# Performance work log

Hardware: AMD Instinct MI355X
Metric: run time of the kernel (lower is better)

Reference implementation:

```python
import jax, jax.numpy as jnp
import numpy as np
import math

N_HEADS = 16
D_EFF = 64
ROPE_BASE = 500.0


def _rope(x, cos, sin):
    # x: (b, h, L, d_eff); cos/sin: (L, d_eff//2)
    x_even = x[..., 0::2]
    x_odd = x[..., 1::2]
    rot = jnp.stack([x_even * cos - x_odd * sin,
                     x_even * sin + x_odd * cos], axis=-1)
    return rot.reshape(x.shape)


def setup_inputs() -> dict:
    key = jax.random.key(0)
    ks = jax.random.split(key, 5)
    B, L, D = 1, 2048, 1024
    X = jax.random.normal(ks[0], (B, L, D), dtype=jnp.float32)
    # causal mask (1 = keep, 0 = masked), broadcastable to (B, h, L, L)
    mask = jnp.tril(jnp.ones((L, L), dtype=jnp.int32))[None, :, :]
    s = 1.0 / math.sqrt(D)
    Wq = jax.random.normal(ks[1], (D, D), dtype=jnp.float32) * s
    Wk = jax.random.normal(ks[2], (D, D), dtype=jnp.float32) * s
    Wv = jax.random.normal(ks[3], (D, D), dtype=jnp.float32) * s
    Wo = jax.random.normal(ks[4], (D, D), dtype=jnp.float32) * s
    return {"X": X, "mask": mask, "Wq": Wq, "Wk": Wk, "Wv": Wv, "Wo": Wo}


def reference(X, mask, Wq, Wk, Wv, Wo):
    b, L, d_model = X.shape
    h, d = N_HEADS, D_EFF
    d_full = h * d

    def split_heads(Y):
        return Y.reshape(b, L, h, d).transpose(0, 2, 1, 3)  # (b,h,L,d)

    Q = split_heads(X @ Wq)
    K = split_heads(X @ Wk)
    V = split_heads(X @ Wv)

    # interleaved RoPE, base 500
    inv_freq = 1.0 / (ROPE_BASE ** (jnp.arange(0, d, 2, dtype=jnp.float32) / d))
    freqs = jnp.arange(L, dtype=jnp.float32)[:, None] * inv_freq  # (L, d/2)
    cos, sin = jnp.cos(freqs), jnp.sin(freqs)
    Q = _rope(Q, cos, sin)
    K = _rope(K, cos, sin)

    S = jnp.einsum('bhqd,bhkd->bhqk', Q, K) / math.sqrt(d)
    S = jnp.where(mask[:, None, :, :] == 0, jnp.float32(-1e9), S)
    # NOTE: faithful to original torch code: softmax over the HEADS axis (dim=1)
    A = jax.nn.softmax(S, axis=1)
    Y = jnp.einsum('bhqk,bhkd->bhqd', A, V)
    Y = Y.transpose(0, 2, 1, 3).reshape(b, L, d_full)
    Y = Y @ Wo
    return Y * math.sqrt(d_model / d_full)
```

## Files before the change

kernel.cpp:

```cpp
#include <hip/hip_runtime.h>
#include <stdint.h>
#include <stddef.h>
#include <math.h>

typedef __attribute__((ext_vector_type(8))) short bf16x8;
typedef __attribute__((ext_vector_type(4))) short short4v;
typedef __attribute__((ext_vector_type(4))) float f32x4;

__device__ __forceinline__ short f2bf(float f) {
  union { float f; uint32_t u; } x; x.f = f;
  return (short)((x.u + 0x7fffu + ((x.u >> 16) & 1u)) >> 16);
}
__device__ __forceinline__ float bf2f(short s) {
  union { uint32_t u; float f; } x; x.u = ((uint32_t)(uint16_t)s) << 16;
  return x.f;
}
__device__ __forceinline__ uint32_t cvt_pk_bf16(float a, float b) {
  uint32_t r;
  asm("v_cvt_pk_bf16_f32 %0, %1, %2" : "=v"(r) : "v"(a), "v"(b));
  return r;
}

__device__ __forceinline__ void gload_lds16(const void* g, void* lds) {
  __builtin_amdgcn_global_load_lds(
      (const __attribute__((address_space(1))) void*)g,
      (__attribute__((address_space(3))) void*)lds, 16, 0, 0);
}

__global__ __launch_bounds__(256) void cast_b(const float* __restrict__ s,
                                              short* __restrict__ d,
                                              float* __restrict__ Cvs) {
  if (blockIdx.x == 0) {
    int c4 = threadIdx.x * 4;
    Cvs[c4] = 0.f; Cvs[c4 + 1] = 0.f; Cvs[c4 + 2] = 0.f; Cvs[c4 + 3] = 0.f;
  }
  int i4 = (blockIdx.x * 256 + threadIdx.x) * 4;
  float4 v = *(const float4*)&s[i4];
  short4v r = { f2bf(v.x), f2bf(v.y), f2bf(v.z), f2bf(v.w) };
  *(short4v*)&d[i4] = r;
}

__global__ __launch_bounds__(256) void reduce_y(const short* __restrict__ Ypc,
                                                const float* __restrict__ Cvs,
                                                short* __restrict__ o) {
  int q = blockIdx.x;
  int j = q >> 5, qr = q & 31;
  int col = threadIdx.x * 4;
  float a0 = Cvs[col + 0], a1 = Cvs[col + 1], a2 = Cvs[col + 2], a3 = Cvs[col + 3];
  int cf = (j - 2) >> 2;
  for (int c = 0; c <= cf; c++) {
    int slot = (c <= 7) ? (c + 8 * (j - 4 * c - 2)) : ((15 - c) + 8 * j);
    const short* p = Ypc + ((size_t)slot * 32 + qr) * 1024 + col;
    short4v v = *(const short4v*)p;
    a0 += bf2f(v[0]); a1 += bf2f(v[1]); a2 += bf2f(v[2]); a3 += bf2f(v[3]);
  }
  if ((j & 3) < 2) {
    int cp = j >> 2;
    int slot = (cp <= 7) ? (cp + 8 * (64 + (j & 3)))
                         : ((15 - cp) + 8 * (66 + (j & 3)));
    const short* p = Ypc + ((size_t)slot * 32 + qr) * 1024 + col;
    short4v v = *(const short4v*)p;
    a0 += bf2f(v[0]); a1 += bf2f(v[1]); a2 += bf2f(v[2]); a3 += bf2f(v[3]);
  }
  uint32_t u0 = cvt_pk_bf16(a0, a1), u1 = cvt_pk_bf16(a2, a3);
  short4v rr = { (short)u0, (short)(u0 >> 16), (short)u1, (short)(u1 >> 16) };
  *(short4v*)&o[(size_t)q * 1024 + col] = rr;
}

__global__ __launch_bounds__(256) void transW(const float* __restrict__ Wq,
                                              const float* __restrict__ Wk,
                                              const float* __restrict__ Wv,
                                              const float* __restrict__ Wo,
                                              short* __restrict__ WcatT,
                                              short* __restrict__ WoT) {
  int z = blockIdx.z;
  const float* src = (z == 0) ? Wq : (z == 1) ? Wk : (z == 2) ? Wv : Wo;
  short* dst = (z == 3) ? WoT : WcatT + (size_t)z * 1024 * 1024;
  __shared__ float tl[32][33];
  int tx = threadIdx.x & 31, ty = threadIdx.x >> 5;
  int kk0 = blockIdx.x * 32;
  int nn0 = blockIdx.y * 32;
#pragma unroll
  for (int j = 0; j < 4; j++)
    tl[ty + j * 8][tx] = src[(size_t)(kk0 + ty + j * 8) * 1024 + nn0 + tx];
  __syncthreads();
#pragma unroll
  for (int j = 0; j < 4; j++)
    dst[(size_t)(nn0 + ty + j * 8) * 1024 + kk0 + tx] = f2bf(tl[tx][ty + j * 8]);
}

__global__ __launch_bounds__(256) void transpose_v(const short* __restrict__ Vb,
                                                   short* __restrict__ Vt,
                                                   float* __restrict__ Cvs) {
  __shared__ short tv[64][72];
  int h = blockIdx.y, k0 = blockIdx.x * 64;
  int tid = threadIdx.x;
#pragma unroll
  for (int j = 0; j < 2; j++) {
    int idx = tid + j * 256;
    int row = idx >> 3, c = idx & 7;
    bf16x8 v = *(const bf16x8*)&Vb[((size_t)h * 2048 + k0 + row) * 64 + c * 8];
#pragma unroll
    for (int t = 0; t < 8; t++) tv[row][c * 8 + t] = v[t];
  }
  __syncthreads();
#pragma unroll
  for (int j = 0; j < 2; j++) {
    int idx = tid + j * 256;
    int d = idx >> 3, c = idx & 7;
    bf16x8 v;
#pragma unroll
    for (int t = 0; t < 8; t++) v[t] = tv[c * 8 + t][d];
    *(bf16x8*)&Vt[((size_t)h * 64 + d) * 2048 + k0 + c * 8] = v;
  }
  if (tid < 64) {
    float s = 0.f;
#pragma unroll 8
    for (int k = 0; k < 64; k++) s += bf2f(tv[k][tid]);
    atomicAdd(&Cvs[h * 64 + tid], s * 0.0625f);
  }
}

template <int MODE>
__global__ __launch_bounds__(256, 2)
void gemm_kernel(const short* __restrict__ A, const short* __restrict__ B,
                 int N, int K, float* __restrict__ C,
                 short* __restrict__ Qb, short* __restrict__ Kb,
                 short* __restrict__ Vb) {
  __shared__ __attribute__((aligned(16))) short lga[128 * 64];
  __shared__ __attribute__((aligned(16))) short lgb[128 * 64];
  const int tid = threadIdx.x;
  const int lane = tid & 63;
  const int w = tid >> 6;
  const int l15 = lane & 15;
  const int quad = lane >> 4;
  const int wm = w >> 1, wn = w & 1;
  const int m0 = blockIdx.x * 128, n0 = blockIdx.y * 128;
  const int rsub = lane >> 3;
  const int cpos = lane & 7;

  f32x4 acc[4][4];
#pragma unroll
  for (int i = 0; i < 4; i++)
#pragma unroll
    for (int j = 0; j < 4; j++) acc[i][j] = (f32x4){0.f, 0.f, 0.f, 0.f};

  for (int kb = 0; kb < K; kb += 64) {
    __syncthreads();
#pragma unroll
    for (int j = 0; j < 4; j++) {
      int r = (w * 4 + j) * 8 + rsub;
      int kc = cpos ^ rsub;
      gload_lds16(A + (size_t)(m0 + r) * K + kb + kc * 8, &lga[(w * 4 + j) * 512]);
      gload_lds16(B + (size_t)(n0 + r) * K + kb + kc * 8, &lgb[(w * 4 + j) * 512]);
    }
    __syncthreads();
#pragma unroll
    for (int kk = 0; kk < 2; kk++) {
      bf16x8 af[4], bfr[4];
#pragma unroll
      for (int t = 0; t < 4; t++) {
        int row = wm * 64 + t * 16 + l15;
        int pc = (kk * 4 + quad) ^ (row & 7);
        af[t] = *(const bf16x8*)&lga[row * 64 + pc * 8];
        int rowb = wn * 64 + t * 16 + l15;
        int pcb = (kk * 4 + quad) ^ (rowb & 7);
        bfr[t] = *(const bf16x8*)&lgb[rowb * 64 + pcb * 8];
      }
#pragma unroll
      for (int mt = 0; mt < 4; mt++)
#pragma unroll
        for (int nt = 0; nt < 4; nt++)
          acc[mt][nt] = __builtin_amdgcn_mfma_f32_16x16x32_bf16(
              af[mt], bfr[nt], acc[mt][nt], 0, 0, 0);
    }
  }

  if (MODE == 0) {
#pragma unroll
    for (int mt = 0; mt < 4; mt++) {
      int q = m0 + wm * 64 + mt * 16 + quad * 4;
#pragma unroll
      for (int nt = 0; nt < 4; nt++) {
        int n = n0 + wn * 64 + nt * 16 + l15;
#pragma unroll
        for (int r = 0; r < 4; r++) C[(size_t)(q + r) * N + n] = acc[mt][nt][r];
      }
    }
  } else {
#pragma unroll
    for (int mt = 0; mt < 4; mt++) {
#pragma unroll
      for (int nt = 0; nt < 4; nt++) {
        int n = n0 + wn * 64 + nt * 16 + l15;
        int mat = n >> 10;
        int h = (n >> 6) & 15;
        int d = n & 63;
#pragma unroll
        for (int r = 0; r < 4; r++) {
          int q = m0 + wm * 64 + mt * 16 + quad * 4 + r;
          float v = acc[mt][nt][r];
          float o = __shfl_xor(v, 1, 64);
          if (mat < 2) {
            int i = d >> 1;
            float ang = (float)q * __builtin_exp2f(-(float)i * 0.2801807588956902f);
            float sn, cs;
            __sincosf(ang, &sn, &cs);
            float rv = (d & 1) ? (o * sn + v * cs) : (v * cs - o * sn);
            short* dst = (mat == 0) ? Qb : Kb;
            dst[((size_t)h * 2048 + q) * 64 + d] = f2bf(rv);
          } else {
            Vb[((size_t)h * 2048 + q) * 64 + d] = f2bf(v);
          }
        }
      }
    }
  }
}

__global__ __launch_bounds__(256, 4)
void gemm_o(const short* __restrict__ A, const short* __restrict__ B,
            float* __restrict__ C) {
  __shared__ __attribute__((aligned(16))) short lga[128 * 64];
  __shared__ __attribute__((aligned(16))) short lgb[64 * 64];
  const int tid = threadIdx.x;
  const int lane = tid & 63;
  const int w = tid >> 6;
  const int l15 = lane & 15;
  const int quad = lane >> 4;
  const int m0 = blockIdx.x * 128, n0 = blockIdx.y * 64;
  const int rsub = lane >> 3;
  const int cpos = lane & 7;

  f32x4 acc[2][4];
#pragma unroll
  for (int i = 0; i < 2; i++)
#pragma unroll
    for (int j = 0; j < 4; j++) acc[i][j] = (f32x4){0.f, 0.f, 0.f, 0.f};

  for (int kb = 0; kb < 1024; kb += 64) {
    __syncthreads();
    int kc = cpos ^ rsub;
#pragma unroll
    for (int j = 0; j < 4; j++) {
      int r = (w * 4 + j) * 8 + rsub;
      gload_lds16(A + (size_t)(m0 + r) * 1024 + kb + kc * 8, &lga[(w * 4 + j) * 512]);
    }
#pragma unroll
    for (int j = 0; j < 2; j++) {
      int r = (w * 2 + j) * 8 + rsub;
      gload_lds16(B + (size_t)(n0 + r) * 1024 + kb + kc * 8, &lgb[(w * 2 + j) * 512]);
    }
    __syncthreads();
#pragma unroll
    for (int kk = 0; kk < 2; kk++) {
      bf16x8 af[2], bfr[4];
#pragma unroll
      for (int t = 0; t < 2; t++) {
        int row = w * 32 + t * 16 + l15;
        int pc = (kk * 4 + quad) ^ (row & 7);
        af[t] = *(const bf16x8*)&lga[row * 64 + pc * 8];
      }
#pragma unroll
      for (int t = 0; t < 4; t++) {
        int rowb = t * 16 + l15;
        int pcb = (kk * 4 + quad) ^ (rowb & 7);
        bfr[t] = *(const bf16x8*)&lgb[rowb * 64 + pcb * 8];
      }
#pragma unroll
      for (int mt = 0; mt < 2; mt++)
#pragma unroll
        for (int nt = 0; nt < 4; nt++)
          acc[mt][nt] = __builtin_amdgcn_mfma_f32_16x16x32_bf16(
              af[mt], bfr[nt], acc[mt][nt], 0, 0, 0);
    }
  }

#pragma unroll
  for (int mt = 0; mt < 2; mt++) {
    int q = m0 + w * 32 + mt * 16 + quad * 4;
#pragma unroll
    for (int nt = 0; nt < 4; nt++) {
      int n = n0 + nt * 16 + l15;
#pragma unroll
      for (int r = 0; r < 4; r++) C[(size_t)(q + r) * 1024 + n] = acc[mt][nt][r];
    }
  }
}

__global__ __launch_bounds__(1024, 2)
void attn_kernel(const short* __restrict__ Qb, const short* __restrict__ Kb,
                 const short* __restrict__ Vt, short* __restrict__ Ypc) {
  __shared__ short Sb[16 * 32 * 72];
  const int tid = threadIdx.x;
  const int lane = tid & 63;
  const int h = tid >> 6;
  const int l15 = lane & 15, quad = lane >> 4;
  const int b = blockIdx.x;
  const int x = b & 7, s = b >> 3;
  int c, j, ng;
  const int n1 = 62 - 4 * x;
  if (s < n1)      { c = x;      j = 4 * x + 2 + s;        ng = 2; }
  else if (s < 64) { c = 15 - x; j = s;                    ng = 2; }
  else if (s < 66) { c = x;      j = 4 * x + (s - 64);     ng = 1; }
  else             { c = 15 - x; j = 60 - 4 * x + (s - 66); ng = 1; }
  const int q0 = j * 32;
  const int g0 = 2 * c;

  bf16x8 qf[2][2];
#pragma unroll
  for (int qs = 0; qs < 2; qs++)
#pragma unroll
    for (int cc = 0; cc < 2; cc++)
      qf[qs][cc] = *(const bf16x8*)&Qb[((size_t)h * 2048 + q0 + qs * 16 + l15) * 64 +
                                       cc * 32 + quad * 8];

  f32x4 yacc[2][4];
#pragma unroll
  for (int i = 0; i < 2; i++)
#pragma unroll
    for (int jj = 0; jj < 4; jj++) yacc[i][jj] = (f32x4){0.f, 0.f, 0.f, 0.f};

  for (int gi = 0; gi < ng; gi++) {
    const int k0 = (g0 + gi) * 64;
#pragma unroll
    for (int st = 0; st < 4; st++) {
      const short* kb = &Kb[((size_t)h * 2048 + k0 + st * 16 + l15) * 64 + quad * 8];
      bf16x8 kf0 = *(const bf16x8*)kb;
      bf16x8 kf1 = *(const bf16x8*)(kb + 32);
#pragma unroll
      for (int qs = 0; qs < 2; qs++) {
        f32x4 sa = (f32x4){0.f, 0.f, 0.f, 0.f};
        sa = __builtin_amdgcn_mfma_f32_16x16x32_bf16(qf[qs][0], kf0, sa, 0, 0, 0);
        sa = __builtin_amdgcn_mfma_f32_16x16x32_bf16(qf[qs][1], kf1, sa, 0, 0, 0);
        const float cs = 0.18033688011112042f;
        uint32_t u0 = cvt_pk_bf16(sa[0] * cs, sa[1] * cs);
        uint32_t u1 = cvt_pk_bf16(sa[2] * cs, sa[3] * cs);
        int rb = (h * 32 + qs * 16 + quad * 4) * 72 + st * 16 + l15;
        Sb[rb]       = (short)u0;
        Sb[rb + 72]  = (short)(u0 >> 16);
        Sb[rb + 144] = (short)u1;
        Sb[rb + 216] = (short)(u1 >> 16);
      }
    }
    __syncthreads();
#pragma unroll
    for (int pp = 0; pp < 2; pp++) {
      int p = tid + pp * 1024;
      int q = p >> 6, kl = p & 63;
      int base = q * 72 + kl;
      float t[16];
      float sum = 0.f;
#pragma unroll
      for (int hh = 0; hh < 16; hh++) {
        float e = __builtin_exp2f(bf2f(Sb[hh * 2304 + base]));
        t[hh] = e;
        sum += e;
      }
      bool msk = (k0 + kl) > (q0 + q);
      float rs = msk ? 0.f : 1.f / sum;
      float offv = msk ? 0.f : 0.0625f;
#pragma unroll
      for (int hh = 0; hh < 16; hh += 2) {
        uint32_t u = cvt_pk_bf16(t[hh] * rs - offv, t[hh + 1] * rs - offv);
        Sb[hh * 2304 + base]       = (short)u;
        Sb[(hh + 1) * 2304 + base] = (short)(u >> 16);
      }
    }
    __syncthreads();
#pragma unroll
    for (int kk = 0; kk < 2; kk++) {
      bf16x8 af0 = *(const bf16x8*)&Sb[(h * 32 + l15) * 72 + kk * 32 + quad * 8];
      bf16x8 af1 = *(const bf16x8*)&Sb[(h * 32 + 16 + l15) * 72 + kk * 32 + quad * 8];
#pragma unroll
      for (int nt = 0; nt < 4; nt++) {
        bf16x8 vf = *(const bf16x8*)&Vt[((size_t)h * 64 + nt * 16 + l15) * 2048 +
                                        k0 + kk * 32 + quad * 8];
        yacc[0][nt] = __builtin_amdgcn_mfma_f32_16x16x32_bf16(af0, vf, yacc[0][nt],
                                                              0, 0, 0);
        yacc[1][nt] = __builtin_amdgcn_mfma_f32_16x16x32_bf16(af1, vf, yacc[1][nt],
                                                              0, 0, 0);
      }
    }
    __syncthreads();
  }
  short* Y = Ypc + (size_t)b * 32 * 1024;
#pragma unroll
  for (int qs = 0; qs < 2; qs++) {
#pragma unroll
    for (int nt = 0; nt < 4; nt++) {
      int col = h * 64 + nt * 16 + l15;
#pragma unroll
      for (int rr = 0; rr < 4; rr++)
        Y[(size_t)(qs * 16 + quad * 4 + rr) * 1024 + col] = f2bf(yacc[qs][nt][rr]);
    }
  }
}

extern "C" void kernel_launch(void* const* d_in, const int* in_sizes, int n_in,
                              void* d_out, int out_size, void* d_ws, size_t ws_size,
                              hipStream_t stream) {
  (void)in_sizes; (void)n_in; (void)out_size; (void)ws_size;
  const float* X  = (const float*)d_in[0];
  const float* Wq = (const float*)d_in[2];
  const float* Wk = (const float*)d_in[3];
  const float* Wv = (const float*)d_in[4];
  const float* Wo = (const float*)d_in[5];
  char* ws = (char*)d_ws;
  const size_t MB = 1024 * 1024;
  short* Xbf   = (short*)(ws + 0);
  short* WcatT = (short*)(ws + 4 * MB);
  short* WoT   = (short*)(ws + 10 * MB);
  short* Qb    = (short*)(ws + 12 * MB);
  short* Kb    = (short*)(ws + 16 * MB);
  short* Vb    = (short*)(ws + 20 * MB);
  short* Vt    = (short*)(ws + 24 * MB);
  short* Ypc   = (short*)(ws + 28 * MB);
  float* Cvs   = (float*)(ws + 63 * MB);
  short* Ycbf  = Xbf;
  float* out   = (float*)d_out;

  cast_b<<<dim3(2048), dim3(256), 0, stream>>>(X, Xbf, Cvs);
  transW<<<dim3(32, 32, 4), dim3(256), 0, stream>>>(Wq, Wk, Wv, Wo, WcatT, WoT);
  gemm_kernel<1><<<dim3(16, 24), dim3(256), 0, stream>>>(Xbf, WcatT, 3072, 1024,
                                                         nullptr, Qb, Kb, Vb);
  transpose_v<<<dim3(32, 16), dim3(256), 0, stream>>>(Vb, Vt, Cvs);
  attn_kernel<<<dim3(544), dim3(1024), 0, stream>>>(Qb, Kb, Vt, Ypc);
  reduce_y<<<dim3(2048), dim3(256), 0, stream>>>(Ypc, Cvs, Ycbf);
  gemm_o<<<dim3(16, 16), dim3(256), 0, stream>>>(Ycbf, WoT, out);
}
```

Measured before the change: 203.6 us.

## Repartition attention into 16-query blocks with 512 threads and 4-chunk key spans

Each attention block now covers 16 query rows instead of 32, using 512 threads where each wave handles two heads. Each block takes up to four 64-key chunks instead of two, and a new block-to-(query, chunk) schedule produces 576 blocks. The partial-output slot mapping and the reduction kernel are rewritten to match. The aim is smaller blocks with more occupancy per CU (launch bounds 512,4) and better load balance across the triangular causal work, at the cost of a different partial-sum count and index arithmetic.

```diff
diff --git a/kernel.cpp b/kernel.cpp
--- a/kernel.cpp
+++ b/kernel.cpp
@@ -44,22 +44,17 @@
                                                 const float* __restrict__ Cvs,
                                                 short* __restrict__ o) {
   int q = blockIdx.x;
-  int j = q >> 5, qr = q & 31;
+  int j = q >> 4, qr = q & 15;
   int col = threadIdx.x * 4;
   float a0 = Cvs[col + 0], a1 = Cvs[col + 1], a2 = Cvs[col + 2], a3 = Cvs[col + 3];
-  int cf = (j - 2) >> 2;
-  for (int c = 0; c <= cf; c++) {
-    int slot = (c <= 7) ? (c + 8 * (j - 4 * c - 2)) : ((15 - c) + 8 * j);
-    const short* p = Ypc + ((size_t)slot * 32 + qr) * 1024 + col;
-    short4v v = *(const short4v*)p;
-    a0 += bf2f(v[0]); a1 += bf2f(v[1]); a2 += bf2f(v[2]); a3 += bf2f(v[3]);
-  }
-  if ((j & 3) < 2) {
-    int cp = j >> 2;
-    int slot = (cp <= 7) ? (cp + 8 * (64 + (j & 3)))
-                         : ((15 - cp) + 8 * (66 + (j & 3)));
-    const short* p = Ypc + ((size_t)slot * 32 + qr) * 1024 + col;
-    short4v v = *(const short4v*)p;
+  int cmax = j >> 4;
+  for (int c = 0; c <= cmax; c++) {
+    int p, t;
+    if (c < 4) { p = c;     t = j - 16 * c; }
+    else       { p = 7 - c; t = j + 16; }
+    int slot = (2 * p + (t & 1)) + 8 * (71 - (t >> 1));
+    const short* pp = Ypc + ((size_t)slot * 16 + qr) * 1024 + col;
+    short4v v = *(const short4v*)pp;
     a0 += bf2f(v[0]); a1 += bf2f(v[1]); a2 += bf2f(v[2]); a3 += bf2f(v[3]);
   }
   uint32_t u0 = cvt_pk_bf16(a0, a1), u1 = cvt_pk_bf16(a2, a3);
@@ -288,31 +283,34 @@
   }
 }
 
-__global__ __launch_bounds__(1024, 2)
+__global__ __launch_bounds__(512, 4)
 void attn_kernel(const short* __restrict__ Qb, const short* __restrict__ Kb,
                  const short* __restrict__ Vt, short* __restrict__ Ypc) {
-  __shared__ short Sb[16 * 32 * 72];
+  __shared__ short Sb[16 * 16 * 72];
   const int tid = threadIdx.x;
   const int lane = tid & 63;
-  const int h = tid >> 6;
+  const int w = tid >> 6;
+  const int h0 = w * 2;
   const int l15 = lane & 15, quad = lane >> 4;
   const int b = blockIdx.x;
-  const int x = b & 7, s = b >> 3;
-  int c, j, ng;
-  const int n1 = 62 - 4 * x;
-  if (s < n1)      { c = x;      j = 4 * x + 2 + s;        ng = 2; }
-  else if (s < 64) { c = 15 - x; j = s;                    ng = 2; }
-  else if (s < 66) { c = x;      j = 4 * x + (s - 64);     ng = 1; }
-  else             { c = 15 - x; j = 60 - 4 * x + (s - 66); ng = 1; }
-  const int q0 = j * 32;
-  const int g0 = 2 * c;
+  const int x = b & 7;
+  const int p = x >> 1;
+  const int t = 2 * (71 - (b >> 3)) + (x & 1);
+  int c, j;
+  if (t < 128 - 16 * p) { c = p;     j = 16 * p + t; }
+  else                  { c = 7 - p; j = t - 16; }
+  const int G = (j >> 2) + 1;
+  const int g0 = 4 * c;
+  int ngt = G - g0;
+  const int ng = (ngt > 4) ? 4 : ngt;
+  const int q0 = j * 16;
 
   bf16x8 qf[2][2];
 #pragma unroll
-  for (int qs = 0; qs < 2; qs++)
+  for (int hh = 0; hh < 2; hh++)
 #pragma unroll
     for (int cc = 0; cc < 2; cc++)
-      qf[qs][cc] = *(const bf16x8*)&Qb[((size_t)h * 2048 + q0 + qs * 16 + l15) * 64 +
+      qf[hh][cc] = *(const bf16x8*)&Qb[((size_t)(h0 + hh) * 2048 + q0 + l15) * 64 +
                                        cc * 32 + quad * 8];
 
   f32x4 yacc[2][4];
@@ -324,19 +322,20 @@
   for (int gi = 0; gi < ng; gi++) {
     const int k0 = (g0 + gi) * 64;
 #pragma unroll
-    for (int st = 0; st < 4; st++) {
-      const short* kb = &Kb[((size_t)h * 2048 + k0 + st * 16 + l15) * 64 + quad * 8];
-      bf16x8 kf0 = *(const bf16x8*)kb;
-      bf16x8 kf1 = *(const bf16x8*)(kb + 32);
-#pragma unroll
-      for (int qs = 0; qs < 2; qs++) {
+    for (int hh = 0; hh < 2; hh++) {
+      int h = h0 + hh;
+#pragma unroll
+      for (int st = 0; st < 4; st++) {
+        const short* kb = &Kb[((size_t)h * 2048 + k0 + st * 16 + l15) * 64 + quad * 8];
+        bf16x8 kf0 = *(const bf16x8*)kb;
+        bf16x8 kf1 = *(const bf16x8*)(kb + 32);
         f32x4 sa = (f32x4){0.f, 0.f, 0.f, 0.f};
-        sa = __builtin_amdgcn_mfma_f32_16x16x32_bf16(qf[qs][0], kf0, sa, 0, 0, 0);
-        sa = __builtin_amdgcn_mfma_f32_16x16x32_bf16(qf[qs][1], kf1, sa, 0, 0, 0);
+        sa = __builtin_amdgcn_mfma_f32_16x16x32_bf16(qf[hh][0], kf0, sa, 0, 0, 0);
+        sa = __builtin_amdgcn_mfma_f32_16x16x32_bf16(qf[hh][1], kf1, sa, 0, 0, 0);
         const float cs = 0.18033688011112042f;
         uint32_t u0 = cvt_pk_bf16(sa[0] * cs, sa[1] * cs);
         uint32_t u1 = cvt_pk_bf16(sa[2] * cs, sa[3] * cs);
-        int rb = (h * 32 + qs * 16 + quad * 4) * 72 + st * 16 + l15;
+        int rb = (h * 16 + quad * 4) * 72 + st * 16 + l15;
         Sb[rb]       = (short)u0;
         Sb[rb + 72]  = (short)(u0 >> 16);
         Sb[rb + 144] = (short)u1;
@@ -346,15 +345,15 @@
     __syncthreads();
 #pragma unroll
     for (int pp = 0; pp < 2; pp++) {
-      int p = tid + pp * 1024;
-      int q = p >> 6, kl = p & 63;
+      int ppos = tid + pp * 512;
+      int q = ppos >> 6, kl = ppos & 63;
       int base = q * 72 + kl;
-      float t[16];
+      float tv[16];
       float sum = 0.f;
 #pragma unroll
       for (int hh = 0; hh < 16; hh++) {
-        float e = __builtin_exp2f(bf2f(Sb[hh * 2304 + base]));
-        t[hh] = e;
+        float e = __builtin_exp2f(bf2f(Sb[hh * 1152 + base]));
+        tv[hh] = e;
         sum += e;
       }
       bool msk = (k0 + kl) > (q0 + q);
@@ -362,37 +361,38 @@
       float offv = msk ? 0.f : 0.0625f;
 #pragma unroll
       for (int hh = 0; hh < 16; hh += 2) {
-        uint32_t u = cvt_pk_bf16(t[hh] * rs - offv, t[hh + 1] * rs - offv);
-        Sb[hh * 2304 + base]       = (short)u;
-        Sb[(hh + 1) * 2304 + base] = (short)(u >> 16);
-      }
-    }
-    __syncthreads();
-#pragma unroll
-    for (int kk = 0; kk < 2; kk++) {
-      bf16x8 af0 = *(const bf16x8*)&Sb[(h * 32 + l15) * 72 + kk * 32 + quad * 8];
-      bf16x8 af1 = *(const bf16x8*)&Sb[(h * 32 + 16 + l15) * 72 + kk * 32 + quad * 8];
-#pragma unroll
-      for (int nt = 0; nt < 4; nt++) {
-        bf16x8 vf = *(const bf16x8*)&Vt[((size_t)h * 64 + nt * 16 + l15) * 2048 +
-                                        k0 + kk * 32 + quad * 8];
-        yacc[0][nt] = __builtin_amdgcn_mfma_f32_16x16x32_bf16(af0, vf, yacc[0][nt],
-                                                              0, 0, 0);
-        yacc[1][nt] = __builtin_amdgcn_mfma_f32_16x16x32_bf16(af1, vf, yacc[1][nt],
-                                                              0, 0, 0);
-      }
-    }
-    __syncthreads();
-  }
-  short* Y = Ypc + (size_t)b * 32 * 1024;
-#pragma unroll
-  for (int qs = 0; qs < 2; qs++) {
+        uint32_t u = cvt_pk_bf16(tv[hh] * rs - offv, tv[hh + 1] * rs - offv);
+        Sb[hh * 1152 + base]       = (short)u;
+        Sb[(hh + 1) * 1152 + base] = (short)(u >> 16);
+      }
+    }
+    __syncthreads();
+#pragma unroll
+    for (int hh = 0; hh < 2; hh++) {
+      int h = h0 + hh;
+#pragma unroll
+      for (int kk = 0; kk < 2; kk++) {
+        bf16x8 af = *(const bf16x8*)&Sb[(h * 16 + l15) * 72 + kk * 32 + quad * 8];
+#pragma unroll
+        for (int nt = 0; nt < 4; nt++) {
+          bf16x8 vf = *(const bf16x8*)&Vt[((size_t)h * 64 + nt * 16 + l15) * 2048 +
+                                          k0 + kk * 32 + quad * 8];
+          yacc[hh][nt] = __builtin_amdgcn_mfma_f32_16x16x32_bf16(af, vf, yacc[hh][nt],
+                                                                 0, 0, 0);
+        }
+      }
+    }
+    __syncthreads();
+  }
+  short* Y = Ypc + (size_t)b * 16 * 1024;
+#pragma unroll
+  for (int hh = 0; hh < 2; hh++) {
 #pragma unroll
     for (int nt = 0; nt < 4; nt++) {
-      int col = h * 64 + nt * 16 + l15;
+      int col = (h0 + hh) * 64 + nt * 16 + l15;
 #pragma unroll
       for (int rr = 0; rr < 4; rr++)
-        Y[(size_t)(qs * 16 + quad * 4 + rr) * 1024 + col] = f2bf(yacc[qs][nt][rr]);
+        Y[(size_t)(quad * 4 + rr) * 1024 + col] = f2bf(yacc[hh][nt][rr]);
     }
   }
 }
@@ -425,7 +425,7 @@
   gemm_kernel<1><<<dim3(16, 24), dim3(256), 0, stream>>>(Xbf, WcatT, 3072, 1024,
                                                          nullptr, Qb, Kb, Vb);
   transpose_v<<<dim3(32, 16), dim3(256), 0, stream>>>(Vb, Vt, Cvs);
-  attn_kernel<<<dim3(544), dim3(1024), 0, stream>>>(Qb, Kb, Vt, Ypc);
+  attn_kernel<<<dim3(576), dim3(512), 0, stream>>>(Qb, Kb, Vt, Ypc);
   reduce_y<<<dim3(2048), dim3(256), 0, stream>>>(Ypc, Cvs, Ycbf);
   gemm_o<<<dim3(16, 16), dim3(256), 0, stream>>>(Ycbf, WoT, out);
 }
```

New measurement: 226.3 us. 11.2% more time.

## Merge cast and weight-transpose kernels; retile QKV GEMM to 128x96 tiles

Applied to the files above, without the earlier changes.

Combines the X bf16 cast and the four weight transposes into one prep kernel, removing a launch. It also specialises the QKV GEMM to fixed K and changes the N tile from 128 to 96, so the grid grows from 384 to 512 blocks and fills more of the CUs. The trade is a smaller per-block N tile, which lowers data reuse per block.

```diff
diff --git a/kernel.cpp b/kernel.cpp
--- a/kernel.cpp
+++ b/kernel.cpp
@@ -27,17 +27,44 @@
       (__attribute__((address_space(3))) void*)lds, 16, 0, 0);
 }
 
-__global__ __launch_bounds__(256) void cast_b(const float* __restrict__ s,
-                                              short* __restrict__ d,
-                                              float* __restrict__ Cvs) {
-  if (blockIdx.x == 0) {
-    int c4 = threadIdx.x * 4;
-    Cvs[c4] = 0.f; Cvs[c4 + 1] = 0.f; Cvs[c4 + 2] = 0.f; Cvs[c4 + 3] = 0.f;
-  }
-  int i4 = (blockIdx.x * 256 + threadIdx.x) * 4;
-  float4 v = *(const float4*)&s[i4];
-  short4v r = { f2bf(v.x), f2bf(v.y), f2bf(v.z), f2bf(v.w) };
-  *(short4v*)&d[i4] = r;
+__global__ __launch_bounds__(256) void prep(const float* __restrict__ X,
+                                            const float* __restrict__ Wq,
+                                            const float* __restrict__ Wk,
+                                            const float* __restrict__ Wv,
+                                            const float* __restrict__ Wo,
+                                            short* __restrict__ Xbf,
+                                            short* __restrict__ WcatT,
+                                            short* __restrict__ WoT,
+                                            float* __restrict__ Cvs) {
+  __shared__ float tl[32][33];
+  int bid = blockIdx.x;
+  if (bid < 2048) {
+    if (bid == 0) {
+      int c4 = threadIdx.x * 4;
+      Cvs[c4] = 0.f; Cvs[c4 + 1] = 0.f; Cvs[c4 + 2] = 0.f; Cvs[c4 + 3] = 0.f;
+    }
+    int i4 = (bid * 256 + threadIdx.x) * 4;
+    float4 v = *(const float4*)&X[i4];
+    short4v r = { f2bf(v.x), f2bf(v.y), f2bf(v.z), f2bf(v.w) };
+    *(short4v*)&Xbf[i4] = r;
+  } else {
+    int wb = bid - 2048;
+    int z = wb >> 10;
+    int bx = (wb >> 5) & 31;
+    int by = wb & 31;
+    const float* src = (z == 0) ? Wq : (z == 1) ? Wk : (z == 2) ? Wv : Wo;
+    short* dst = (z == 3) ? WoT : WcatT + (size_t)z * 1024 * 1024;
+    int tx = threadIdx.x & 31, ty = threadIdx.x >> 5;
+    int kk0 = bx * 32;
+    int nn0 = by * 32;
+#pragma unroll
+    for (int j = 0; j < 4; j++)
+      tl[ty + j * 8][tx] = src[(size_t)(kk0 + ty + j * 8) * 1024 + nn0 + tx];
+    __syncthreads();
+#pragma unroll
+    for (int j = 0; j < 4; j++)
+      dst[(size_t)(nn0 + ty + j * 8) * 1024 + kk0 + tx] = f2bf(tl[tx][ty + j * 8]);
+  }
 }
 
 __global__ __launch_bounds__(256) void reduce_y(const short* __restrict__ Ypc,
@@ -67,28 +94,6 @@
   *(short4v*)&o[(size_t)q * 1024 + col] = rr;
 }
 
-__global__ __launch_bounds__(256) void transW(const float* __restrict__ Wq,
-                                              const float* __restrict__ Wk,
-                                              const float* __restrict__ Wv,
-                                              const float* __restrict__ Wo,
-                                              short* __restrict__ WcatT,
-                                              short* __restrict__ WoT) {
-  int z = blockIdx.z;
-  const float* src = (z == 0) ? Wq : (z == 1) ? Wk : (z == 2) ? Wv : Wo;
-  short* dst = (z == 3) ? WoT : WcatT + (size_t)z * 1024 * 1024;
-  __shared__ float tl[32][33];
-  int tx = threadIdx.x & 31, ty = threadIdx.x >> 5;
-  int kk0 = blockIdx.x * 32;
-  int nn0 = blockIdx.y * 32;
-#pragma unroll
-  for (int j = 0; j < 4; j++)
-    tl[ty + j * 8][tx] = src[(size_t)(kk0 + ty + j * 8) * 1024 + nn0 + tx];
-  __syncthreads();
-#pragma unroll
-  for (int j = 0; j < 4; j++)
-    dst[(size_t)(nn0 + ty + j * 8) * 1024 + kk0 + tx] = f2bf(tl[tx][ty + j * 8]);
-}
-
 __global__ __launch_bounds__(256) void transpose_v(const short* __restrict__ Vb,
                                                    short* __restrict__ Vt,
                                                    float* __restrict__ Cvs) {
@@ -121,97 +126,89 @@
   }
 }
 
-template <int MODE>
 __global__ __launch_bounds__(256, 2)
-void gemm_kernel(const short* __restrict__ A, const short* __restrict__ B,
-                 int N, int K, float* __restrict__ C,
-                 short* __restrict__ Qb, short* __restrict__ Kb,
-                 short* __restrict__ Vb) {
+void gemm_qkv(const short* __restrict__ A, const short* __restrict__ B,
+              short* __restrict__ Qb, short* __restrict__ Kb,
+              short* __restrict__ Vb) {
   __shared__ __attribute__((aligned(16))) short lga[128 * 64];
-  __shared__ __attribute__((aligned(16))) short lgb[128 * 64];
+  __shared__ __attribute__((aligned(16))) short lgb[96 * 64];
   const int tid = threadIdx.x;
   const int lane = tid & 63;
   const int w = tid >> 6;
   const int l15 = lane & 15;
   const int quad = lane >> 4;
   const int wm = w >> 1, wn = w & 1;
-  const int m0 = blockIdx.x * 128, n0 = blockIdx.y * 128;
+  const int m0 = blockIdx.x * 128, n0 = blockIdx.y * 96;
   const int rsub = lane >> 3;
   const int cpos = lane & 7;
 
-  f32x4 acc[4][4];
+  f32x4 acc[4][3];
 #pragma unroll
   for (int i = 0; i < 4; i++)
 #pragma unroll
-    for (int j = 0; j < 4; j++) acc[i][j] = (f32x4){0.f, 0.f, 0.f, 0.f};
-
-  for (int kb = 0; kb < K; kb += 64) {
-    __syncthreads();
+    for (int j = 0; j < 3; j++) acc[i][j] = (f32x4){0.f, 0.f, 0.f, 0.f};
+
+  for (int kb = 0; kb < 1024; kb += 64) {
+    __syncthreads();
+    int kc = cpos ^ rsub;
 #pragma unroll
     for (int j = 0; j < 4; j++) {
       int r = (w * 4 + j) * 8 + rsub;
-      int kc = cpos ^ rsub;
-      gload_lds16(A + (size_t)(m0 + r) * K + kb + kc * 8, &lga[(w * 4 + j) * 512]);
-      gload_lds16(B + (size_t)(n0 + r) * K + kb + kc * 8, &lgb[(w * 4 + j) * 512]);
+      gload_lds16(A + (size_t)(m0 + r) * 1024 + kb + kc * 8, &lga[(w * 4 + j) * 512]);
+    }
+#pragma unroll
+    for (int j = 0; j < 3; j++) {
+      int r = (w * 3 + j) * 8 + rsub;
+      gload_lds16(B + (size_t)(n0 + r) * 1024 + kb + kc * 8, &lgb[(w * 3 + j) * 512]);
     }
     __syncthreads();
 #pragma unroll
     for (int kk = 0; kk < 2; kk++) {
-      bf16x8 af[4], bfr[4];
+      bf16x8 af[4], bfr[3];
 #pragma unroll
       for (int t = 0; t < 4; t++) {
         int row = wm * 64 + t * 16 + l15;
         int pc = (kk * 4 + quad) ^ (row & 7);
         af[t] = *(const bf16x8*)&lga[row * 64 + pc * 8];
-        int rowb = wn * 64 + t * 16 + l15;
+      }
+#pragma unroll
+      for (int t = 0; t < 3; t++) {
+        int rowb = wn * 48 + t * 16 + l15;
         int pcb = (kk * 4 + quad) ^ (rowb & 7);
         bfr[t] = *(const bf16x8*)&lgb[rowb * 64 + pcb * 8];
       }
 #pragma unroll
       for (int mt = 0; mt < 4; mt++)
 #pragma unroll
-        for (int nt = 0; nt < 4; nt++)
+        for (int nt = 0; nt < 3; nt++)
           acc[mt][nt] = __builtin_amdgcn_mfma_f32_16x16x32_bf16(
               af[mt], bfr[nt], acc[mt][nt], 0, 0, 0);
     }
   }
 
-  if (MODE == 0) {
-#pragma unroll
-    for (int mt = 0; mt < 4; mt++) {
-      int q = m0 + wm * 64 + mt * 16 + quad * 4;
-#pragma unroll
-      for (int nt = 0; nt < 4; nt++) {
-        int n = n0 + wn * 64 + nt * 16 + l15;
-#pragma unroll
-        for (int r = 0; r < 4; r++) C[(size_t)(q + r) * N + n] = acc[mt][nt][r];
-      }
-    }
-  } else {
-#pragma unroll
-    for (int mt = 0; mt < 4; mt++) {
-#pragma unroll
-      for (int nt = 0; nt < 4; nt++) {
-        int n = n0 + wn * 64 + nt * 16 + l15;
-        int mat = n >> 10;
-        int h = (n >> 6) & 15;
-        int d = n & 63;
-#pragma unroll
-        for (int r = 0; r < 4; r++) {
-          int q = m0 + wm * 64 + mt * 16 + quad * 4 + r;
-          float v = acc[mt][nt][r];
-          float o = __shfl_xor(v, 1, 64);
-          if (mat < 2) {
-            int i = d >> 1;
-            float ang = (float)q * __builtin_exp2f(-(float)i * 0.2801807588956902f);
-            float sn, cs;
-            __sincosf(ang, &sn, &cs);
-            float rv = (d & 1) ? (o * sn + v * cs) : (v * cs - o * sn);
-            short* dst = (mat == 0) ? Qb : Kb;
-            dst[((size_t)h * 2048 + q) * 64 + d] = f2bf(rv);
-          } else {
-            Vb[((size_t)h * 2048 + q) * 64 + d] = f2bf(v);
-          }
+#pragma unroll
+  for (int mt = 0; mt < 4; mt++) {
+#pragma unroll
+    for (int nt = 0; nt < 3; nt++) {
+      int n = n0 + wn * 48 + nt * 16 + l15;
+      int mat = n >> 10;
+      int h = (n >> 6) & 15;
+      int d = n & 63;
+#pragma unroll
+      for (int r = 0; r < 4; r++) {
+        int q = m0 + wm * 64 + mt * 16 + quad * 4 + r;
+        float v = acc[mt][nt][r];
+        float o = __shfl_xor(v, 1, 64);
+        if (mat < 2) {
+          int i = d >> 1;
+          float ang = (float)q * __builtin_exp2f(-(float)i * 0.2801807588956902f);
+          float sn, cs;
+          __sincosf(ang, &sn, &cs);
+          float rv = (d & 1) ? (o * sn + v * cs) : (v * cs - o * sn);
+          short* dst = (mat == 0) ? Qb : Kb;
+          dst[((size_t)h * 2048 + q) * 64 + d] = f2bf(rv);
+        } else {
+          Vb[((size_t)h * 2048 + q) * 64 + d] = f2bf(v);
         }
       }
     }
@@ -420,10 +417,8 @@
   short* Ycbf  = Xbf;
   float* out   = (float*)d_out;
 
-  cast_b<<<dim3(2048), dim3(256), 0, stream>>>(X, Xbf, Cvs);
-  transW<<<dim3(32, 32, 4), dim3(256), 0, stream>>>(Wq, Wk, Wv, Wo, WcatT, WoT);
-  gemm_kernel<1><<<dim3(16, 24), dim3(256), 0, stream>>>(Xbf, WcatT, 3072, 1024,
-                                                         nullptr, Qb, Kb, Vb);
+  prep<<<dim3(6144), dim3(256), 0, stream>>>(X, Wq, Wk, Wv, Wo, Xbf, WcatT, WoT, Cvs);
+  gemm_qkv<<<dim3(16, 32), dim3(256), 0, stream>>>(Xbf, WcatT, Qb, Kb, Vb);
   transpose_v<<<dim3(32, 16), dim3(256), 0, stream>>>(Vb, Vt, Cvs);
   attn_kernel<<<dim3(544), dim3(1024), 0, stream>>>(Qb, Kb, Vt, Ypc);
   reduce_y<<<dim3(2048), dim3(256), 0, stream>>>(Ypc, Cvs, Ycbf);
```

Result: faster. 199.4 us (-2.0%).
